# Performance work log

Hardware: AMD Instinct MI355X
Metric: run time of the kernel (lower is better)

Reference implementation:

```python
import jax, jax.numpy as jnp
import numpy as np

EPS = 1e-6

def _ln2d(x, g, b):
    # x: [b,H,W,c]; LayerNorm2d normalizes over channel dim per spatial location
    mu = jnp.mean(x, axis=-1, keepdims=True)
    var = jnp.mean((x - mu) ** 2, axis=-1, keepdims=True)
    return (x - mu) * jax.lax.rsqrt(var + EPS) * g + b

def _proj(x, w, b):
    # 1x1 conv == channel matmul; w: [c_out, c_in]
    return jnp.einsum('bhwc,dc->bhwd', x, w) + b

def setup_inputs() -> dict:
    key = jax.random.key(0)
    ks = jax.random.split(key, 16)
    b, c, H, W = 8, 96, 128, 256
    s = 0.02
    return {
        'feat_l': jax.random.normal(ks[0], (b, H * W, c), jnp.float32),
        'feat_r': jax.random.normal(ks[1], (b, H * W, c), jnp.float32),
        'g_nl': jnp.ones((c,), jnp.float32),
        'b_nl': jnp.zeros((c,), jnp.float32),
        'g_nr': jnp.ones((c,), jnp.float32),
        'b_nr': jnp.zeros((c,), jnp.float32),
        'w_l1': jax.random.normal(ks[2], (c, c), jnp.float32) * s,
        'bias_l1': jax.random.normal(ks[3], (c,), jnp.float32) * s,
        'w_r1': jax.random.normal(ks[4], (c, c), jnp.float32) * s,
        'bias_r1': jax.random.normal(ks[5], (c,), jnp.float32) * s,
        'w_l2': jax.random.normal(ks[6], (c, c), jnp.float32) * s,
        'bias_l2': jax.random.normal(ks[7], (c,), jnp.float32) * s,
        'w_r2': jax.random.normal(ks[8], (c, c), jnp.float32) * s,
        'bias_r2': jax.random.normal(ks[9], (c,), jnp.float32) * s,
        'beta': jax.random.normal(ks[10], (c,), jnp.float32) * 0.1,
        'gamma': jax.random.normal(ks[11], (c,), jnp.float32) * 0.1,
        'H': 128,
        'W': 256,
    }

def reference(feat_l, feat_r, g_nl, b_nl, g_nr, b_nr,
              w_l1, bias_l1, w_r1, bias_r1, w_l2, bias_l2, w_r2, bias_r2,
              beta, gamma, H, W):
    b, _, c = feat_l.shape
    scale = c ** (-0.5)
    # work in channels-last [b,H,W,c] (equivalent to torch's NCHW + permutes)
    x_l = feat_l.reshape(b, H, W, c)
    x_r = feat_r.reshape(b, H, W, c)
    Q_l = _proj(_ln2d(x_l, g_nl, b_nl), w_l1, bias_l1)   # [b,H,W,c]
    Q_r = _proj(_ln2d(x_r, g_nr, b_nr), w_r1, bias_r1)   # [b,H,W,c]
    V_l = _proj(x_l, w_l2, bias_l2)
    V_r = _proj(x_r, w_r2, bias_r2)
    attn = jnp.einsum('bhwc,bhvc->bhwv', Q_l, Q_r) * scale  # [b,H,W_l,W_r]
    F_r2l = jnp.einsum('bhwv,bhvc->bhwc', jax.nn.softmax(attn, axis=-1), V_r)
    attn_t = jnp.swapaxes(attn, -1, -2)                      # [b,H,W_r,W_l]
    F_l2r = jnp.einsum('bhvw,bhwc->bhvc', jax.nn.softmax(attn_t, axis=-1), V_l)
    out_l = x_l + F_r2l * beta
    out_r = x_r + F_l2r * gamma
    return (out_l.reshape(b, H * W, c), out_r.reshape(b, H * W, c))
```

## Files before the change

### kernel.cpp

```cpp
#include <hip/hip_runtime.h>
#include <stdint.h>

#define C96   96
#define TOTEL 25165824L

typedef __attribute__((ext_vector_type(16))) float f32x16;
typedef __attribute__((ext_vector_type(8)))  short short8;

#define QL_OFF  0
#define QR_OFF  53248
#define XT0_OFF 106496
#define XT1_OFF 119808
#define VT0_OFF 133120
#define VT1_OFF 146944
#define W1Q_OFF 106496
#define W1K_OFF 126464
#define LDS_SZ  160768

#define MFMA32(a,b,c) __builtin_amdgcn_mfma_f32_32x32x16_bf16(a,b,c,0,0,0)

__device__ __forceinline__ uint32_t cvtpk(float lo, float hi) {
    uint32_t d;
    asm("v_cvt_pk_bf16_f32 %0, %1, %2" : "=v"(d) : "v"(lo), "v"(hi));
    return d;
}
__device__ __forceinline__ float bl(uint32_t u){ union{uint32_t i;float f;}a; a.i=u<<16;        return a.f; }
__device__ __forceinline__ float bh(uint32_t u){ union{uint32_t i;float f;}a; a.i=u&0xffff0000u; return a.f; }

union F8 { uint32_t u[4]; short8 s; uint4 q; };

template<int ITERS>
__device__ __forceinline__ void stage(const float* __restrict__ src, char* dst, int t) {
#pragma unroll
    for (int i = 0; i < ITERS; ++i) {
        const int idx4 = i * 512 + t;
        const float4 v = *(const float4*)(src + (size_t)idx4 * 4);
        const int r = idx4 / 24;
        const int c = (idx4 % 24) * 4;
        uint2 p; p.x = cvtpk(v.x, v.y); p.y = cvtpk(v.z, v.w);
        *(uint2*)(dst + r * 208 + c * 2) = p;
    }
}

__device__ __forceinline__ void stageW(const float* __restrict__ W, char* dst, int t) {
#pragma unroll
    for (int i = 0; i < 5; ++i) {
        const int idx4 = i * 512 + t;
        if (idx4 < 2304) {
            const float4 v = *(const float4*)(W + (size_t)idx4 * 4);
            const int r = idx4 / 24;
            const int c = (idx4 % 24) * 4;
            uint2 p; p.x = cvtpk(v.x, v.y); p.y = cvtpk(v.z, v.w);
            *(uint2*)(dst + r * 208 + c * 2) = p;
        }
    }
}

__device__ __forceinline__ void stats512(char* lds_, int t) {
    char* row = lds_ + ((t < 256) ? QL_OFF : QR_OFF) + (t & 255) * 208;
    float sm = 0.f, s2 = 0.f;
#pragma unroll
    for (int i = 0; i < 12; ++i) {
        F8 w; w.q = *(const uint4*)(row + i * 16);
#pragma unroll
        for (int j = 0; j < 4; ++j) {
            const float a = bl(w.u[j]), b = bh(w.u[j]);
            sm += a + b; s2 += a * a + b * b;
        }
    }
    const float mu = sm * (1.f / 96.f);
    float var = s2 * (1.f / 96.f) - mu * mu;
    var = fmaxf(var, 0.f);
    *(float2*)(row + 192) = make_float2(mu, rsqrtf(var + 1e-6f));
}

__device__ __forceinline__ void proj_inplace(char* lds_, int qoff, int woff,
    const float* __restrict__ gv, const float* __restrict__ bv,
    const float* __restrict__ bias1, float outscale, int wv, int l31, int s)
{
    char* row = lds_ + qoff + (wv * 32 + l31) * 208;
    const float2 st = *(const float2*)(row + 192);
    const float mu = st.x, rs = st.y;
    short8 bf[6];
#pragma unroll
    for (int kf = 0; kf < 6; ++kf) {
        const int c0 = kf * 16 + s * 8;
        F8 raw; raw.q = *(const uint4*)(row + c0 * 2);
        const float4 g0 = *(const float4*)(gv + c0);
        const float4 g1 = *(const float4*)(gv + c0 + 4);
        const float4 b0 = *(const float4*)(bv + c0);
        const float4 b1 = *(const float4*)(bv + c0 + 4);
        const float x0=bl(raw.u[0]),x1=bh(raw.u[0]),x2=bl(raw.u[1]),x3=bh(raw.u[1]);
        const float x4=bl(raw.u[2]),x5=bh(raw.u[2]),x6=bl(raw.u[3]),x7=bh(raw.u[3]);
        F8 o;
        o.u[0] = cvtpk((x0-mu)*rs*g0.x + b0.x, (x1-mu)*rs*g0.y + b0.y);
        o.u[1] = cvtpk((x2-mu)*rs*g0.z + b0.z, (x3-mu)*rs*g0.w + b0.w);
        o.u[2] = cvtpk((x4-mu)*rs*g1.x + b1.x, (x5-mu)*rs*g1.y + b1.y);
        o.u[3] = cvtpk((x6-mu)*rs*g1.z + b1.z, (x7-mu)*rs*g1.w + b1.w);
        bf[kf] = o.s;
    }
    f32x16 qa[3];
#pragma unroll
    for (int i = 0; i < 16; ++i) { qa[0][i] = 0.f; qa[1][i] = 0.f; qa[2][i] = 0.f; }
#pragma unroll
    for (int kf = 0; kf < 6; ++kf) {
#pragma unroll
        for (int mf = 0; mf < 3; ++mf) {
            const short8 af = *(const short8*)(lds_ + woff + (mf * 32 + l31) * 208 + kf * 32 + s * 16);
            qa[mf] = MFMA32(af, bf[kf], qa[mf]);
        }
    }
#pragma unroll
    for (int mf = 0; mf < 3; ++mf) {
#pragma unroll
        for (int blk = 0; blk < 4; ++blk) {
            const int d = mf * 32 + blk * 8 + s * 4;
            const float4 bb = *(const float4*)(bias1 + d);
            uint2 p;
            p.x = cvtpk((qa[mf][blk*4+0] + bb.x) * outscale, (qa[mf][blk*4+1] + bb.y) * outscale);
            p.y = cvtpk((qa[mf][blk*4+2] + bb.z) * outscale, (qa[mf][blk*4+3] + bb.w) * outscale);
            *(uint2*)(row + d * 2) = p;
        }
    }
}

__device__ __forceinline__ void vproj(char* lds_, int xt_off, int vt_off,
    const short8* wf, const float* __restrict__ B2, int mfv, int nfv, int l31, int s)
{
    f32x16 va;
#pragma unroll
    for (int i = 0; i < 16; ++i) va[i] = 0.f;
#pragma unroll
    for (int kf = 0; kf < 6; ++kf) {
        const short8 xb = *(const short8*)(lds_ + xt_off + (nfv * 32 + l31) * 208 + kf * 32 + s * 16);
        va = MFMA32(wf[kf], xb, va);
    }
    const int v = nfv * 32 + l31;
#pragma unroll
    for (int blk = 0; blk < 4; ++blk) {
        const int d = mfv * 32 + blk * 8 + s * 4;
        const float4 bb = *(const float4*)(B2 + d);
        *(uint16_t*)(lds_ + vt_off + (d+0) * 144 + v * 2) = (uint16_t)cvtpk(va[blk*4+0] + bb.x, 0.f);
        *(uint16_t*)(lds_ + vt_off + (d+1) * 144 + v * 2) = (uint16_t)cvtpk(va[blk*4+1] + bb.y, 0.f);
        *(uint16_t*)(lds_ + vt_off + (d+2) * 144 + v * 2) = (uint16_t)cvtpk(va[blk*4+2] + bb.z, 0.f);
        *(uint16_t*)(lds_ + vt_off + (d+3) * 144 + v * 2) = (uint16_t)cvtpk(va[blk*4+3] + bb.w, 0.f);
    }
}

__device__ __forceinline__ void scalc(const char* lds_, int koff, int vt,
                                      const short8* bq, int l31, int s, f32x16* sa)
{
#pragma unroll
    for (int i = 0; i < 16; ++i) { sa[0][i] = 0.f; sa[1][i] = 0.f; }
#pragma unroll
    for (int kf = 0; kf < 6; ++kf) {
        const short8 a0 = *(const short8*)(lds_ + koff + (vt * 64 +      l31) * 208 + kf * 32 + s * 16);
        const short8 a1 = *(const short8*)(lds_ + koff + (vt * 64 + 32 + l31) * 208 + kf * 32 + s * 16);
        sa[0] = MFMA32(a0, bq[kf], sa[0]);
        sa[1] = MFMA32(a1, bq[kf], sa[1]);
    }
}

extern "C" __global__ __launch_bounds__(512, 2) void scam_fused(
    const float* __restrict__ feat_l, const float* __restrict__ feat_r,
    const float* __restrict__ g_nl, const float* __restrict__ b_nl,
    const float* __restrict__ g_nr, const float* __restrict__ b_nr,
    const float* __restrict__ w_l1, const float* __restrict__ bias_l1,
    const float* __restrict__ w_r1, const float* __restrict__ bias_r1,
    const float* __restrict__ w_l2, const float* __restrict__ bias_l2,
    const float* __restrict__ w_r2, const float* __restrict__ bias_r2,
    const float* __restrict__ beta, const float* __restrict__ gamma,
    float* __restrict__ out)
{
    extern __shared__ char lds[];
    const int t    = threadIdx.x;
    const int wv   = t >> 6;
    const int lane = t & 63;
    const int l31  = lane & 31;
    const int s    = lane >> 5;
    const size_t eb = (size_t)blockIdx.x * (256 * C96);
    const float scale = 0.10206207261596577f;

    stage<12>(feat_l + eb, lds + QL_OFF, t);
    stage<12>(feat_r + eb, lds + QR_OFF, t);
    stageW(w_l1, lds + (0 ? W1K_OFF : W1Q_OFF), t);
    stageW(w_r1, lds + W1K_OFF, t);
    __syncthreads();
    stats512(lds, t);
    __syncthreads();
    proj_inplace(lds, QL_OFF, W1Q_OFF, g_nl, b_nl, bias_l1, scale, wv, l31, s);
    proj_inplace(lds, QR_OFF, W1K_OFF, g_nr, b_nr, bias_r1, 1.0f,  wv, l31, s);

    for (int dir = 0; dir < 2; ++dir) {
        const int qoff = dir ? QR_OFF : QL_OFF;
        const int koff = dir ? QL_OFF : QR_OFF;
        const float* Xk   = dir ? feat_l  : feat_r;
        const float* Xq   = dir ? feat_r  : feat_l;
        const float* W2   = dir ? w_l2    : w_r2;
        const float* B2   = dir ? bias_l2 : bias_r2;
        const float* mixv = dir ? gamma   : beta;

        short8 bq[6];
#pragma unroll
        for (int kf = 0; kf < 6; ++kf)
            bq[kf] = *(const short8*)(lds + qoff + (wv * 32 + l31) * 208 + kf * 32 + s * 16);

        short8 wf[6];
        const int mfv = wv % 3, nfv = wv / 3;
        if (wv < 6) {
#pragma unroll
            for (int kf = 0; kf < 6; ++kf) {
                const float* wp = W2 + (mfv * 32 + l31) * 96 + kf * 16 + s * 8;
                const float4 a0 = *(const float4*)wp;
                const float4 a1 = *(const float4*)(wp + 4);
                F8 af;
                af.u[0] = cvtpk(a0.x, a0.y); af.u[1] = cvtpk(a0.z, a0.w);
                af.u[2] = cvtpk(a1.x, a1.y); af.u[3] = cvtpk(a1.z, a1.w);
                wf[kf] = af.s;
            }
        }

        f32x16 O[3];
#pragma unroll
        for (int i = 0; i < 16; ++i) { O[0][i] = 0.f; O[1][i] = 0.f; O[2][i] = 0.f; }
        float m_run = -1e30f, l_run = 0.f;
        f32x16 sab[2][2];

        __syncthreads();
        stage<3>(Xk + eb, lds + XT0_OFF, t);
        __syncthreads();
        if (wv < 6) vproj(lds, XT0_OFF, VT0_OFF, wf, B2, mfv, nfv, l31, s);
        stage<3>(Xk + eb + 64 * 96, lds + XT1_OFF, t);
        __syncthreads();
        scalc(lds, koff, 0, bq, l31, s, sab[0]);

#pragma unroll
        for (int vt = 0; vt < 4; ++vt) {
            const int cb = vt & 1, nb = cb ^ 1;
            if (vt < 3) scalc(lds, koff, vt + 1, bq, l31, s, sab[nb]);

            f32x16* sa = sab[cb];
            float tm = -1e30f;
#pragma unroll
            for (int i = 0; i < 16; ++i) { tm = fmaxf(tm, sa[0][i]); tm = fmaxf(tm, sa[1][i]); }
            tm = fmaxf(tm, __shfl_xor(tm, 32));
            const float mn = fmaxf(m_run, tm);
            const float al = __expf(m_run - mn);
            float ps = 0.f;
#pragma unroll
            for (int i = 0; i < 16; ++i) {
                sa[0][i] = __expf(sa[0][i] - mn); ps += sa[0][i];
                sa[1][i] = __expf(sa[1][i] - mn); ps += sa[1][i];
            }
            ps += __shfl_xor(ps, 32);
            l_run = l_run * al + ps;
            m_run = mn;
            O[0] *= al; O[1] *= al; O[2] *= al;

            const int vtoff = cb ? VT1_OFF : VT0_OFF;
#pragma unroll
            for (int kk = 0; kk < 4; ++kk) {
                const int mf = kk >> 1, base = (kk & 1) * 8;
                const uint32_t A0 = cvtpk(sa[mf][base+0], sa[mf][base+1]);
                const uint32_t A1 = cvtpk(sa[mf][base+2], sa[mf][base+3]);
                const uint32_t B0 = cvtpk(sa[mf][base+4], sa[mf][base+5]);
                const uint32_t B1 = cvtpk(sa[mf][base+6], sa[mf][base+7]);
                const uint32_t rA0 = __shfl_xor(A0, 32);
                const uint32_t rA1 = __shfl_xor(A1, 32);
                const uint32_t rB0 = __shfl_xor(B0, 32);
                const uint32_t rB1 = __shfl_xor(B1, 32);
                F8 pb;
                pb.u[0] = s ? rB0 : A0;
                pb.u[1] = s ? rB1 : A1;
                pb.u[2] = s ? B0  : rA0;
                pb.u[3] = s ? B1  : rA1;
#pragma unroll
                for (int mf2 = 0; mf2 < 3; ++mf2) {
                    const short8 av = *(const short8*)(lds + vtoff + (mf2 * 32 + l31) * 144 + kk * 32 + s * 16);
                    O[mf2] = MFMA32(av, pb.s, O[mf2]);
                }
            }

            if (vt < 3) {
                __syncthreads();
                if (wv < 6) vproj(lds, nb ? XT1_OFF : XT0_OFF, nb ? VT1_OFF : VT0_OFF,
                                  wf, B2, mfv, nfv, l31, s);
                if (vt < 2) stage<3>(Xk + eb + (size_t)(vt + 2) * 64 * 96,
                                     lds + (cb ? XT1_OFF : XT0_OFF), t);
                __syncthreads();
            }
        }

        const float inv = 1.f / l_run;
        const size_t rowbase = eb + (size_t)(wv * 32 + l31) * 96;
        float* oo = out + (dir ? TOTEL : 0);
#pragma unroll
        for (int mf = 0; mf < 3; ++mf) {
#pragma unroll
            for (int blk = 0; blk < 4; ++blk) {
                const int d = mf * 32 + blk * 8 + s * 4;
                const float4 mx = *(const float4*)(mixv + d);
                const float4 xr = *(const float4*)(Xq + rowbase + d);
                float4 ov;
                ov.x = fmaf(O[mf][blk*4+0] * inv, mx.x, xr.x);
                ov.y = fmaf(O[mf][blk*4+1] * inv, mx.y, xr.y);
                ov.z = fmaf(O[mf][blk*4+2] * inv, mx.z, xr.z);
                ov.w = fmaf(O[mf][blk*4+3] * inv, mx.w, xr.w);
                *(float4*)(oo + rowbase + d) = ov;
            }
        }
    }
}

extern "C" void kernel_launch(void* const* d_in, const int* in_sizes, int n_in,
                              void* d_out, int out_size, void* d_ws, size_t ws_size,
                              hipStream_t stream) {
    const float* feat_l  = (const float*)d_in[0];
    const float* feat_r  = (const float*)d_in[1];
    const float* g_nl    = (const float*)d_in[2];
    const float* b_nl    = (const float*)d_in[3];
    const float* g_nr    = (const float*)d_in[4];
    const float* b_nr    = (const float*)d_in[5];
    const float* w_l1    = (const float*)d_in[6];
    const float* bias_l1 = (const float*)d_in[7];
    const float* w_r1    = (const float*)d_in[8];
    const float* bias_r1 = (const float*)d_in[9];
    const float* w_l2    = (const float*)d_in[10];
    const float* bias_l2 = (const float*)d_in[11];
    const float* w_r2    = (const float*)d_in[12];
    const float* bias_r2 = (const float*)d_in[13];
    const float* beta    = (const float*)d_in[14];
    const float* gamma   = (const float*)d_in[15];
    float* out = (float*)d_out;

    hipLaunchKernelGGL(scam_fused, dim3(1024), dim3(512), LDS_SZ, stream,
                       feat_l, feat_r, g_nl, b_nl, g_nr, b_nr,
                       w_l1, bias_l1, w_r1, bias_r1, w_l2, bias_l2, w_r2, bias_r2,
                       beta, gamma, out);
}
```

Measured before the change: 215.2 us.

## Software-pipeline attention loop with register-staged loads, exp2 softmax, lazy rescale, setprio

Unrolls the four-tile attention loop by hand and splits global staging into issue and commit steps, so loads of the next K/V tile are in flight during score computation, softmax and the PV matmul. This cuts the barriers per tile from two to one. Softmax now uses the raw v_exp_f32 instruction, with log2(e) folded into the Q scale, and skips the running-max rescale of O when the new max grows by at most 8. MFMA blocks are wrapped in s_setprio, and the residual input rows are prefetched before the last PV. The costs are higher register pressure from the held float4 loads and the xr prefetch, plus a new barrier after projection.

```diff
diff --git a/kernel.cpp b/kernel.cpp
--- a/kernel.cpp
+++ b/kernel.cpp
@@ -24,32 +24,49 @@
     asm("v_cvt_pk_bf16_f32 %0, %1, %2" : "=v"(d) : "v"(lo), "v"(hi));
     return d;
 }
+__device__ __forceinline__ float fexp2(float x) {
+    float r; asm("v_exp_f32 %0, %1" : "=v"(r) : "v"(x)); return r;
+}
 __device__ __forceinline__ float bl(uint32_t u){ union{uint32_t i;float f;}a; a.i=u<<16;        return a.f; }
 __device__ __forceinline__ float bh(uint32_t u){ union{uint32_t i;float f;}a; a.i=u&0xffff0000u; return a.f; }
 
 union F8 { uint32_t u[4]; short8 s; uint4 q; };
 
+__device__ __forceinline__ void stage_issue(const float* __restrict__ src, int t,
+                                            float4& a0, float4& a1, float4& a2) {
+    a0 = *(const float4*)(src + (size_t)(0 * 512 + t) * 4);
+    a1 = *(const float4*)(src + (size_t)(1 * 512 + t) * 4);
+    a2 = *(const float4*)(src + (size_t)(2 * 512 + t) * 4);
+}
+__device__ __forceinline__ void stage_commit(char* dst, int t,
+                                             const float4& a0, const float4& a1, const float4& a2) {
+#pragma unroll
+    for (int i = 0; i < 3; ++i) {
+        const float4 v = (i == 0) ? a0 : (i == 1) ? a1 : a2;
+        const int idx4 = i * 512 + t;
+        const int r = idx4 / 24, c = (idx4 % 24) * 4;
+        uint2 p; p.x = cvtpk(v.x, v.y); p.y = cvtpk(v.z, v.w);
+        *(uint2*)(dst + r * 208 + c * 2) = p;
+    }
+}
 template<int ITERS>
 __device__ __forceinline__ void stage(const float* __restrict__ src, char* dst, int t) {
 #pragma unroll
     for (int i = 0; i < ITERS; ++i) {
         const int idx4 = i * 512 + t;
         const float4 v = *(const float4*)(src + (size_t)idx4 * 4);
-        const int r = idx4 / 24;
-        const int c = (idx4 % 24) * 4;
+        const int r = idx4 / 24, c = (idx4 % 24) * 4;
         uint2 p; p.x = cvtpk(v.x, v.y); p.y = cvtpk(v.z, v.w);
         *(uint2*)(dst + r * 208 + c * 2) = p;
     }
 }
-
 __device__ __forceinline__ void stageW(const float* __restrict__ W, char* dst, int t) {
 #pragma unroll
     for (int i = 0; i < 5; ++i) {
         const int idx4 = i * 512 + t;
         if (idx4 < 2304) {
             const float4 v = *(const float4*)(W + (size_t)idx4 * 4);
-            const int r = idx4 / 24;
-            const int c = (idx4 % 24) * 4;
+            const int r = idx4 / 24, c = (idx4 % 24) * 4;
             uint2 p; p.x = cvtpk(v.x, v.y); p.y = cvtpk(v.z, v.w);
             *(uint2*)(dst + r * 208 + c * 2) = p;
         }
@@ -102,6 +119,7 @@
     f32x16 qa[3];
 #pragma unroll
     for (int i = 0; i < 16; ++i) { qa[0][i] = 0.f; qa[1][i] = 0.f; qa[2][i] = 0.f; }
+    __builtin_amdgcn_s_setprio(1);
 #pragma unroll
     for (int kf = 0; kf < 6; ++kf) {
 #pragma unroll
@@ -110,6 +128,7 @@
             qa[mf] = MFMA32(af, bf[kf], qa[mf]);
         }
     }
+    __builtin_amdgcn_s_setprio(0);
 #pragma unroll
     for (int mf = 0; mf < 3; ++mf) {
 #pragma unroll
@@ -130,11 +149,13 @@
     f32x16 va;
 #pragma unroll
     for (int i = 0; i < 16; ++i) va[i] = 0.f;
+    __builtin_amdgcn_s_setprio(1);
 #pragma unroll
     for (int kf = 0; kf < 6; ++kf) {
         const short8 xb = *(const short8*)(lds_ + xt_off + (nfv * 32 + l31) * 208 + kf * 32 + s * 16);
         va = MFMA32(wf[kf], xb, va);
     }
+    __builtin_amdgcn_s_setprio(0);
     const int v = nfv * 32 + l31;
 #pragma unroll
     for (int blk = 0; blk < 4; ++blk) {
@@ -152,6 +173,7 @@
 {
 #pragma unroll
     for (int i = 0; i < 16; ++i) { sa[0][i] = 0.f; sa[1][i] = 0.f; }
+    __builtin_amdgcn_s_setprio(1);
 #pragma unroll
     for (int kf = 0; kf < 6; ++kf) {
         const short8 a0 = *(const short8*)(lds_ + koff + (vt * 64 +      l31) * 208 + kf * 32 + s * 16);
@@ -159,6 +181,87 @@
         sa[0] = MFMA32(a0, bq[kf], sa[0]);
         sa[1] = MFMA32(a1, bq[kf], sa[1]);
     }
+    __builtin_amdgcn_s_setprio(0);
+}
+
+__device__ __forceinline__ void softmax_tile(f32x16* sa, f32x16* O, float& m_run, float& l_run)
+{
+    float t0=-1e30f,t1=-1e30f,t2=-1e30f,t3=-1e30f;
+#pragma unroll
+    for (int i = 0; i < 16; i += 4) {
+        t0 = fmaxf(t0, fmaxf(sa[0][i+0], sa[1][i+0]));
+        t1 = fmaxf(t1, fmaxf(sa[0][i+1], sa[1][i+1]));
+        t2 = fmaxf(t2, fmaxf(sa[0][i+2], sa[1][i+2]));
+        t3 = fmaxf(t3, fmaxf(sa[0][i+3], sa[1][i+3]));
+    }
+    float tm = fmaxf(fmaxf(t0,t1), fmaxf(t2,t3));
+    tm = fmaxf(tm, __shfl_xor(tm, 32));
+    if (__all(tm - m_run <= 8.f)) {
+        const float mb = m_run;
+        float p0=0.f,p1=0.f,p2=0.f,p3=0.f;
+#pragma unroll
+        for (int i = 0; i < 16; i += 4) {
+            sa[0][i+0]=fexp2(sa[0][i+0]-mb); p0+=sa[0][i+0];
+            sa[1][i+0]=fexp2(sa[1][i+0]-mb); p0+=sa[1][i+0];
+            sa[0][i+1]=fexp2(sa[0][i+1]-mb); p1+=sa[0][i+1];
+            sa[1][i+1]=fexp2(sa[1][i+1]-mb); p1+=sa[1][i+1];
+            sa[0][i+2]=fexp2(sa[0][i+2]-mb); p2+=sa[0][i+2];
+            sa[1][i+2]=fexp2(sa[1][i+2]-mb); p2+=sa[1][i+2];
+            sa[0][i+3]=fexp2(sa[0][i+3]-mb); p3+=sa[0][i+3];
+            sa[1][i+3]=fexp2(sa[1][i+3]-mb); p3+=sa[1][i+3];
+        }
+        float ps = (p0+p1)+(p2+p3);
+        ps += __shfl_xor(ps, 32);
+        l_run += ps;
+    } else {
+        const float mn = fmaxf(m_run, tm);
+        const float al = fexp2(m_run - mn);
+        float p0=0.f,p1=0.f,p2=0.f,p3=0.f;
+#pragma unroll
+        for (int i = 0; i < 16; i += 4) {
+            sa[0][i+0]=fexp2(sa[0][i+0]-mn); p0+=sa[0][i+0];
+            sa[1][i+0]=fexp2(sa[1][i+0]-mn); p0+=sa[1][i+0];
+            sa[0][i+1]=fexp2(sa[0][i+1]-mn); p1+=sa[0][i+1];
+            sa[1][i+1]=fexp2(sa[1][i+1]-mn); p1+=sa[1][i+1];
+            sa[0][i+2]=fexp2(sa[0][i+2]-mn); p2+=sa[0][i+2];
+            sa[1][i+2]=fexp2(sa[1][i+2]-mn); p2+=sa[1][i+2];
+            sa[0][i+3]=fexp2(sa[0][i+3]-mn); p3+=sa[0][i+3];
+            sa[1][i+3]=fexp2(sa[1][i+3]-mn); p3+=sa[1][i+3];
+        }
+        float ps = (p0+p1)+(p2+p3);
+        ps += __shfl_xor(ps, 32);
+        l_run = l_run * al + ps;
+        m_run = mn;
+        O[0] *= al; O[1] *= al; O[2] *= al;
+    }
+}
+
+__device__ __forceinline__ void pv(const char* lds_, int vtoff, f32x16* sa, f32x16* O, int l31, int s)
+{
+    __builtin_amdgcn_s_setprio(1);
+#pragma unroll
+    for (int kk = 0; kk < 4; ++kk) {
+        const int mf = kk >> 1, base = (kk & 1) * 8;
+        const uint32_t A0 = cvtpk(sa[mf][base+0], sa[mf][base+1]);
+        const uint32_t A1 = cvtpk(sa[mf][base+2], sa[mf][base+3]);
+        const uint32_t B0 = cvtpk(sa[mf][base+4], sa[mf][base+5]);
+        const uint32_t B1 = cvtpk(sa[mf][base+6], sa[mf][base+7]);
+        const uint32_t rA0 = __shfl_xor(A0, 32);
+        const uint32_t rA1 = __shfl_xor(A1, 32);
+        const uint32_t rB0 = __shfl_xor(B0, 32);
+        const uint32_t rB1 = __shfl_xor(B1, 32);
+        F8 pb;
+        pb.u[0] = s ? rB0 : A0;
+        pb.u[1] = s ? rB1 : A1;
+        pb.u[2] = s ? B0  : rA0;
+        pb.u[3] = s ? B1  : rA1;
+#pragma unroll
+        for (int mf2 = 0; mf2 < 3; ++mf2) {
+            const short8 av = *(const short8*)(lds_ + vtoff + (mf2 * 32 + l31) * 144 + kk * 32 + s * 16);
+            O[mf2] = MFMA32(av, pb.s, O[mf2]);
+        }
+    }
+    __builtin_amdgcn_s_setprio(0);
 }
 
 extern "C" __global__ __launch_bounds__(512, 2) void scam_fused(
@@ -179,17 +282,18 @@
     const int l31  = lane & 31;
     const int s    = lane >> 5;
     const size_t eb = (size_t)blockIdx.x * (256 * C96);
-    const float scale = 0.10206207261596577f;
+    const float scale = 0.10206207261596577f * 1.4426950408889634f;
 
     stage<12>(feat_l + eb, lds + QL_OFF, t);
     stage<12>(feat_r + eb, lds + QR_OFF, t);
-    stageW(w_l1, lds + (0 ? W1K_OFF : W1Q_OFF), t);
+    stageW(w_l1, lds + W1Q_OFF, t);
     stageW(w_r1, lds + W1K_OFF, t);
     __syncthreads();
     stats512(lds, t);
     __syncthreads();
     proj_inplace(lds, QL_OFF, W1Q_OFF, g_nl, b_nl, bias_l1, scale, wv, l31, s);
     proj_inplace(lds, QR_OFF, W1K_OFF, g_nr, b_nr, bias_r1, 1.0f,  wv, l31, s);
+    __syncthreads();
 
     for (int dir = 0; dir < 2; ++dir) {
         const int qoff = dir ? QR_OFF : QL_OFF;
@@ -199,6 +303,9 @@
         const float* W2   = dir ? w_l2    : w_r2;
         const float* B2   = dir ? bias_l2 : bias_r2;
         const float* mixv = dir ? gamma   : beta;
+
+        float4 A0, A1, A2;
+        stage_issue(Xk + eb, t, A0, A1, A2);
 
         short8 bq[6];
 #pragma unroll
@@ -220,79 +327,50 @@
             }
         }
 
+        stage_commit(lds + XT0_OFF, t, A0, A1, A2);
+        __syncthreads();
+        if (wv < 6) vproj(lds, XT0_OFF, VT0_OFF, wf, B2, mfv, nfv, l31, s);
+        stage_issue(Xk + eb + 64 * 96, t, A0, A1, A2);
+        stage_commit(lds + XT1_OFF, t, A0, A1, A2);
+        __syncthreads();
+
         f32x16 O[3];
 #pragma unroll
         for (int i = 0; i < 16; ++i) { O[0][i] = 0.f; O[1][i] = 0.f; O[2][i] = 0.f; }
         float m_run = -1e30f, l_run = 0.f;
-        f32x16 sab[2][2];
-
+        f32x16 sa0[2], sa1[2];
+        scalc(lds, koff, 0, bq, l31, s, sa0);
+
+        stage_issue(Xk + eb + 2 * 64 * 96, t, A0, A1, A2);
+        scalc(lds, koff, 1, bq, l31, s, sa1);
+        softmax_tile(sa0, O, m_run, l_run);
+        if (wv < 6) vproj(lds, XT1_OFF, VT1_OFF, wf, B2, mfv, nfv, l31, s);
+        pv(lds, VT0_OFF, sa0, O, l31, s);
+        stage_commit(lds + XT0_OFF, t, A0, A1, A2);
         __syncthreads();
-        stage<3>(Xk + eb, lds + XT0_OFF, t);
+        stage_issue(Xk + eb + 3 * 64 * 96, t, A0, A1, A2);
+        scalc(lds, koff, 2, bq, l31, s, sa0);
+        softmax_tile(sa1, O, m_run, l_run);
+        if (wv < 6) vproj(lds, XT0_OFF, VT0_OFF, wf, B2, mfv, nfv, l31, s);
+        pv(lds, VT1_OFF, sa1, O, l31, s);
+        stage_commit(lds + XT1_OFF, t, A0, A1, A2);
         __syncthreads();
-        if (wv < 6) vproj(lds, XT0_OFF, VT0_OFF, wf, B2, mfv, nfv, l31, s);
-        stage<3>(Xk + eb + 64 * 96, lds + XT1_OFF, t);
+        scalc(lds, koff, 3, bq, l31, s, sa1);
+        softmax_tile(sa0, O, m_run, l_run);
+        if (wv < 6) vproj(lds, XT1_OFF, VT1_OFF, wf, B2, mfv, nfv, l31, s);
+        pv(lds, VT0_OFF, sa0, O, l31, s);
         __syncthreads();
-        scalc(lds, koff, 0, bq, l31, s, sab[0]);
-
-#pragma unroll
-        for (int vt = 0; vt < 4; ++vt) {
-            const int cb = vt & 1, nb = cb ^ 1;
-            if (vt < 3) scalc(lds, koff, vt + 1, bq, l31, s, sab[nb]);
-
-            f32x16* sa = sab[cb];
-            float tm = -1e30f;
-#pragma unroll
-            for (int i = 0; i < 16; ++i) { tm = fmaxf(tm, sa[0][i]); tm = fmaxf(tm, sa[1][i]); }
-            tm = fmaxf(tm, __shfl_xor(tm, 32));
-            const float mn = fmaxf(m_run, tm);
-            const float al = __expf(m_run - mn);
-            float ps = 0.f;
-#pragma unroll
-            for (int i = 0; i < 16; ++i) {
-                sa[0][i] = __expf(sa[0][i] - mn); ps += sa[0][i];
-                sa[1][i] = __expf(sa[1][i] - mn); ps += sa[1][i];
-            }
-            ps += __shfl_xor(ps, 32);
-            l_run = l_run * al + ps;
-            m_run = mn;
-            O[0] *= al; O[1] *= al; O[2] *= al;
-
-            const int vtoff = cb ? VT1_OFF : VT0_OFF;
-#pragma unroll
-            for (int kk = 0; kk < 4; ++kk) {
-                const int mf = kk >> 1, base = (kk & 1) * 8;
-                const uint32_t A0 = cvtpk(sa[mf][base+0], sa[mf][base+1]);
-                const uint32_t A1 = cvtpk(sa[mf][base+2], sa[mf][base+3]);
-                const uint32_t B0 = cvtpk(sa[mf][base+4], sa[mf][base+5]);
-                const uint32_t B1 = cvtpk(sa[mf][base+6], sa[mf][base+7]);
-                const uint32_t rA0 = __shfl_xor(A0, 32);
-                const uint32_t rA1 = __shfl_xor(A1, 32);
-                const uint32_t rB0 = __shfl_xor(B0, 32);
-                const uint32_t rB1 = __shfl_xor(B1, 32);
-                F8 pb;
-                pb.u[0] = s ? rB0 : A0;
-                pb.u[1] = s ? rB1 : A1;
-                pb.u[2] = s ? B0  : rA0;
-                pb.u[3] = s ? B1  : rA1;
-#pragma unroll
-                for (int mf2 = 0; mf2 < 3; ++mf2) {
-                    const short8 av = *(const short8*)(lds + vtoff + (mf2 * 32 + l31) * 144 + kk * 32 + s * 16);
-                    O[mf2] = MFMA32(av, pb.s, O[mf2]);
-                }
-            }
-
-            if (vt < 3) {
-                __syncthreads();
-                if (wv < 6) vproj(lds, nb ? XT1_OFF : XT0_OFF, nb ? VT1_OFF : VT0_OFF,
-                                  wf, B2, mfv, nfv, l31, s);
-                if (vt < 2) stage<3>(Xk + eb + (size_t)(vt + 2) * 64 * 96,
-                                     lds + (cb ? XT1_OFF : XT0_OFF), t);
-                __syncthreads();
-            }
-        }
+        softmax_tile(sa1, O, m_run, l_run);
+        const size_t rowbase = eb + (size_t)(wv * 32 + l31) * 96;
+        float4 xr[12];
+#pragma unroll
+        for (int mf = 0; mf < 3; ++mf)
+#pragma unroll
+            for (int blk = 0; blk < 4; ++blk)
+                xr[mf*4+blk] = *(const float4*)(Xq + rowbase + mf * 32 + blk * 8 + s * 4);
+        pv(lds, VT1_OFF, sa1, O, l31, s);
 
         const float inv = 1.f / l_run;
-        const size_t rowbase = eb + (size_t)(wv * 32 + l31) * 96;
         float* oo = out + (dir ? TOTEL : 0);
 #pragma unroll
         for (int mf = 0; mf < 3; ++mf) {
@@ -300,12 +378,12 @@
             for (int blk = 0; blk < 4; ++blk) {
                 const int d = mf * 32 + blk * 8 + s * 4;
                 const float4 mx = *(const float4*)(mixv + d);
-                const float4 xr = *(const float4*)(Xq + rowbase + d);
+                const float4 rv = xr[mf*4+blk];
                 float4 ov;
-                ov.x = fmaf(O[mf][blk*4+0] * inv, mx.x, xr.x);
-                ov.y = fmaf(O[mf][blk*4+1] * inv, mx.y, xr.y);
-                ov.z = fmaf(O[mf][blk*4+2] * inv, mx.z, xr.z);
-                ov.w = fmaf(O[mf][blk*4+3] * inv, mx.w, xr.w);
+                ov.x = fmaf(O[mf][blk*4+0] * inv, mx.x, rv.x);
+                ov.y = fmaf(O[mf][blk*4+1] * inv, mx.y, rv.y);
+                ov.z = fmaf(O[mf][blk*4+2] * inv, mx.z, rv.z);
+                ov.w = fmaf(O[mf][blk*4+3] * inv, mx.w, rv.w);
                 *(float4*)(oo + rowbase + d) = ov;
             }
         }
```

New measurement: 296.0 us. +37.5%, slower.

## Use exp2 softmax with deferred max rescale and MFMA priority hints

Applied to the files above, without the earlier changes.

Folds log2(e) into the query projection scale so the online softmax can call the raw v_exp_f32 (base-2) instruction instead of __expf. It skips the running-max update and the O/l rescale when no lane's tile max exceeds the running max by more than 8. It also splits the max and sum reductions into four independent chains and wraps the MFMA loops with s_setprio so matrix work gets issue priority over other waves. Deferring the rescale leaves exponentials up to 2^8 in bf16 P and fp32 accumulators, which is safe for these magnitudes but slightly changes numerics.

```diff
diff --git a/kernel.cpp b/kernel.cpp
--- a/kernel.cpp
+++ b/kernel.cpp
@@ -24,6 +24,9 @@
     asm("v_cvt_pk_bf16_f32 %0, %1, %2" : "=v"(d) : "v"(lo), "v"(hi));
     return d;
 }
+__device__ __forceinline__ float fexp2(float x) {
+    float r; asm("v_exp_f32 %0, %1" : "=v"(r) : "v"(x)); return r;
+}
 __device__ __forceinline__ float bl(uint32_t u){ union{uint32_t i;float f;}a; a.i=u<<16;        return a.f; }
 __device__ __forceinline__ float bh(uint32_t u){ union{uint32_t i;float f;}a; a.i=u&0xffff0000u; return a.f; }
 
@@ -35,21 +38,18 @@
     for (int i = 0; i < ITERS; ++i) {
         const int idx4 = i * 512 + t;
         const float4 v = *(const float4*)(src + (size_t)idx4 * 4);
-        const int r = idx4 / 24;
-        const int c = (idx4 % 24) * 4;
+        const int r = idx4 / 24, c = (idx4 % 24) * 4;
         uint2 p; p.x = cvtpk(v.x, v.y); p.y = cvtpk(v.z, v.w);
         *(uint2*)(dst + r * 208 + c * 2) = p;
     }
 }
-
 __device__ __forceinline__ void stageW(const float* __restrict__ W, char* dst, int t) {
 #pragma unroll
     for (int i = 0; i < 5; ++i) {
         const int idx4 = i * 512 + t;
         if (idx4 < 2304) {
             const float4 v = *(const float4*)(W + (size_t)idx4 * 4);
-            const int r = idx4 / 24;
-            const int c = (idx4 % 24) * 4;
+            const int r = idx4 / 24, c = (idx4 % 24) * 4;
             uint2 p; p.x = cvtpk(v.x, v.y); p.y = cvtpk(v.z, v.w);
             *(uint2*)(dst + r * 208 + c * 2) = p;
         }
@@ -102,6 +102,7 @@
     f32x16 qa[3];
 #pragma unroll
     for (int i = 0; i < 16; ++i) { qa[0][i] = 0.f; qa[1][i] = 0.f; qa[2][i] = 0.f; }
+    __builtin_amdgcn_s_setprio(1);
 #pragma unroll
     for (int kf = 0; kf < 6; ++kf) {
 #pragma unroll
@@ -110,6 +111,7 @@
             qa[mf] = MFMA32(af, bf[kf], qa[mf]);
         }
     }
+    __builtin_amdgcn_s_setprio(0);
 #pragma unroll
     for (int mf = 0; mf < 3; ++mf) {
 #pragma unroll
@@ -130,11 +132,13 @@
     f32x16 va;
 #pragma unroll
     for (int i = 0; i < 16; ++i) va[i] = 0.f;
+    __builtin_amdgcn_s_setprio(1);
 #pragma unroll
     for (int kf = 0; kf < 6; ++kf) {
         const short8 xb = *(const short8*)(lds_ + xt_off + (nfv * 32 + l31) * 208 + kf * 32 + s * 16);
         va = MFMA32(wf[kf], xb, va);
     }
+    __builtin_amdgcn_s_setprio(0);
     const int v = nfv * 32 + l31;
 #pragma unroll
     for (int blk = 0; blk < 4; ++blk) {
@@ -152,6 +156,7 @@
 {
 #pragma unroll
     for (int i = 0; i < 16; ++i) { sa[0][i] = 0.f; sa[1][i] = 0.f; }
+    __builtin_amdgcn_s_setprio(1);
 #pragma unroll
     for (int kf = 0; kf < 6; ++kf) {
         const short8 a0 = *(const short8*)(lds_ + koff + (vt * 64 +      l31) * 208 + kf * 32 + s * 16);
@@ -159,6 +164,73 @@
         sa[0] = MFMA32(a0, bq[kf], sa[0]);
         sa[1] = MFMA32(a1, bq[kf], sa[1]);
     }
+    __builtin_amdgcn_s_setprio(0);
+}
+
+__device__ __forceinline__ void softmax_tile(f32x16* sa, f32x16* O, float& m_run, float& l_run)
+{
+    float t0=-1e30f,t1=-1e30f,t2=-1e30f,t3=-1e30f;
+#pragma unroll
+    for (int i = 0; i < 16; i += 4) {
+        t0 = fmaxf(t0, fmaxf(sa[0][i+0], sa[1][i+0]));
+        t1 = fmaxf(t1, fmaxf(sa[0][i+1], sa[1][i+1]));
+        t2 = fmaxf(t2, fmaxf(sa[0][i+2], sa[1][i+2]));
+        t3 = fmaxf(t3, fmaxf(sa[0][i+3], sa[1][i+3]));
+    }
+    float tm = fmaxf(fmaxf(t0,t1), fmaxf(t2,t3));
+    tm = fmaxf(tm, __shfl_xor(tm, 32));
+    const bool defer = __all(tm - m_run <= 8.f);
+    const float mn = defer ? m_run : fmaxf(m_run, tm);
+    float p0=0.f,p1=0.f,p2=0.f,p3=0.f;
+#pragma unroll
+    for (int i = 0; i < 16; i += 4) {
+        sa[0][i+0]=fexp2(sa[0][i+0]-mn); p0+=sa[0][i+0];
+        sa[1][i+0]=fexp2(sa[1][i+0]-mn); p0+=sa[1][i+0];
+        sa[0][i+1]=fexp2(sa[0][i+1]-mn); p1+=sa[0][i+1];
+        sa[1][i+1]=fexp2(sa[1][i+1]-mn); p1+=sa[1][i+1];
+        sa[0][i+2]=fexp2(sa[0][i+2]-mn); p2+=sa[0][i+2];
+        sa[1][i+2]=fexp2(sa[1][i+2]-mn); p2+=sa[1][i+2];
+        sa[0][i+3]=fexp2(sa[0][i+3]-mn); p3+=sa[0][i+3];
+        sa[1][i+3]=fexp2(sa[1][i+3]-mn); p3+=sa[1][i+3];
+    }
+    float ps = (p0+p1)+(p2+p3);
+    ps += __shfl_xor(ps, 32);
+    if (defer) {
+        l_run += ps;
+    } else {
+        const float al = fexp2(m_run - mn);
+        l_run = l_run * al + ps;
+        m_run = mn;
+        O[0] *= al; O[1] *= al; O[2] *= al;
+    }
+}
+
+__device__ __forceinline__ void pv(const char* lds_, int vtoff, f32x16* sa, f32x16* O, int l31, int s)
+{
+    __builtin_amdgcn_s_setprio(1);
+#pragma unroll
+    for (int kk = 0; kk < 4; ++kk) {
+        const int mf = kk >> 1, base = (kk & 1) * 8;
+        const uint32_t A0 = cvtpk(sa[mf][base+0], sa[mf][base+1]);
+        const uint32_t A1 = cvtpk(sa[mf][base+2], sa[mf][base+3]);
+        const uint32_t B0 = cvtpk(sa[mf][base+4], sa[mf][base+5]);
+        const uint32_t B1 = cvtpk(sa[mf][base+6], sa[mf][base+7]);
+        const uint32_t rA0 = __shfl_xor(A0, 32);
+        const uint32_t rA1 = __shfl_xor(A1, 32);
+        const uint32_t rB0 = __shfl_xor(B0, 32);
+        const uint32_t rB1 = __shfl_xor(B1, 32);
+        F8 pb;
+        pb.u[0] = s ? rB0 : A0;
+        pb.u[1] = s ? rB1 : A1;
+        pb.u[2] = s ? B0  : rA0;
+        pb.u[3] = s ? B1  : rA1;
+#pragma unroll
+        for (int mf2 = 0; mf2 < 3; ++mf2) {
+            const short8 av = *(const short8*)(lds_ + vtoff + (mf2 * 32 + l31) * 144 + kk * 32 + s * 16);
+            O[mf2] = MFMA32(av, pb.s, O[mf2]);
+        }
+    }
+    __builtin_amdgcn_s_setprio(0);
 }
 
 extern "C" __global__ __launch_bounds__(512, 2) void scam_fused(
@@ -179,11 +251,11 @@
     const int l31  = lane & 31;
     const int s    = lane >> 5;
     const size_t eb = (size_t)blockIdx.x * (256 * C96);
-    const float scale = 0.10206207261596577f;
+    const float scale = 0.10206207261596577f * 1.4426950408889634f;
 
     stage<12>(feat_l + eb, lds + QL_OFF, t);
     stage<12>(feat_r + eb, lds + QR_OFF, t);
-    stageW(w_l1, lds + (0 ? W1K_OFF : W1Q_OFF), t);
+    stageW(w_l1, lds + W1Q_OFF, t);
     stageW(w_r1, lds + W1K_OFF, t);
     __syncthreads();
     stats512(lds, t);
@@ -240,46 +312,9 @@
             if (vt < 3) scalc(lds, koff, vt + 1, bq, l31, s, sab[nb]);
 
             f32x16* sa = sab[cb];
-            float tm = -1e30f;
-#pragma unroll
-            for (int i = 0; i < 16; ++i) { tm = fmaxf(tm, sa[0][i]); tm = fmaxf(tm, sa[1][i]); }
-            tm = fmaxf(tm, __shfl_xor(tm, 32));
-            const float mn = fmaxf(m_run, tm);
-            const float al = __expf(m_run - mn);
-            float ps = 0.f;
-#pragma unroll
-            for (int i = 0; i < 16; ++i) {
-                sa[0][i] = __expf(sa[0][i] - mn); ps += sa[0][i];
-                sa[1][i] = __expf(sa[1][i] - mn); ps += sa[1][i];
-            }
-            ps += __shfl_xor(ps, 32);
-            l_run = l_run * al + ps;
-            m_run = mn;
-            O[0] *= al; O[1] *= al; O[2] *= al;
-
-            const int vtoff = cb ? VT1_OFF : VT0_OFF;
-#pragma unroll
-            for (int kk = 0; kk < 4; ++kk) {
-                const int mf = kk >> 1, base = (kk & 1) * 8;
-                const uint32_t A0 = cvtpk(sa[mf][base+0], sa[mf][base+1]);
-                const uint32_t A1 = cvtpk(sa[mf][base+2], sa[mf][base+3]);
-                const uint32_t B0 = cvtpk(sa[mf][base+4], sa[mf][base+5]);
-                const uint32_t B1 = cvtpk(sa[mf][base+6], sa[mf][base+7]);
-                const uint32_t rA0 = __shfl_xor(A0, 32);
-                const uint32_t rA1 = __shfl_xor(A1, 32);
-                const uint32_t rB0 = __shfl_xor(B0, 32);
-                const uint32_t rB1 = __shfl_xor(B1, 32);
-                F8 pb;
-                pb.u[0] = s ? rB0 : A0;
-                pb.u[1] = s ? rB1 : A1;
-                pb.u[2] = s ? B0  : rA0;
-                pb.u[3] = s ? B1  : rA1;
-#pragma unroll
-                for (int mf2 = 0; mf2 < 3; ++mf2) {
-                    const short8 av = *(const short8*)(lds + vtoff + (mf2 * 32 + l31) * 144 + kk * 32 + s * 16);
-                    O[mf2] = MFMA32(av, pb.s, O[mf2]);
-                }
-            }
+            softmax_tile(sa, O, m_run, l_run);
+
+            pv(lds, cb ? VT1_OFF : VT0_OFF, sa, O, l31, s);
 
             if (vt < 3) {
                 __syncthreads();
```

After: 226.4 us. 1.05x slower.

## Compute full V projection upfront from global memory, drop pipelined staging

Applied to the files above, without the earlier changes.

Instead of double-buffering 64-row tiles of the key-side input through LDS and computing V projections tile by tile between softmax steps, each direction now computes the full 256-row V^T into a single LDS buffer at the start. The work is spread across all 8 waves, with X and W read directly from global memory. The attention loop then processes 32-key halves with no barriers inside. This removes several __syncthreads per direction and the idle waves during vproj. In exchange it loses the overlap of V computation with attention, and the score accumulator shrinks to one tile per step, which may reduce MFMA ILP.

```diff
diff --git a/kernel.cpp b/kernel.cpp
--- a/kernel.cpp
+++ b/kernel.cpp
@@ -7,15 +7,14 @@
 typedef __attribute__((ext_vector_type(16))) float f32x16;
 typedef __attribute__((ext_vector_type(8)))  short short8;
 
-#define QL_OFF  0
-#define QR_OFF  53248
-#define XT0_OFF 106496
-#define XT1_OFF 119808
-#define VT0_OFF 133120
-#define VT1_OFF 146944
+#define QROWB  208
+#define VROWB  528
+#define QL_OFF 0
+#define QR_OFF 53248
+#define VT_OFF 106496
 #define W1Q_OFF 106496
 #define W1K_OFF 126464
-#define LDS_SZ  160768
+#define LDS_SZ 157184
 
 #define MFMA32(a,b,c) __builtin_amdgcn_mfma_f32_32x32x16_bf16(a,b,c,0,0,0)
 
@@ -35,29 +34,26 @@
     for (int i = 0; i < ITERS; ++i) {
         const int idx4 = i * 512 + t;
         const float4 v = *(const float4*)(src + (size_t)idx4 * 4);
-        const int r = idx4 / 24;
-        const int c = (idx4 % 24) * 4;
+        const int r = idx4 / 24, c = (idx4 % 24) * 4;
         uint2 p; p.x = cvtpk(v.x, v.y); p.y = cvtpk(v.z, v.w);
-        *(uint2*)(dst + r * 208 + c * 2) = p;
-    }
-}
-
+        *(uint2*)(dst + r * QROWB + c * 2) = p;
+    }
+}
 __device__ __forceinline__ void stageW(const float* __restrict__ W, char* dst, int t) {
 #pragma unroll
     for (int i = 0; i < 5; ++i) {
         const int idx4 = i * 512 + t;
         if (idx4 < 2304) {
             const float4 v = *(const float4*)(W + (size_t)idx4 * 4);
-            const int r = idx4 / 24;
-            const int c = (idx4 % 24) * 4;
+            const int r = idx4 / 24, c = (idx4 % 24) * 4;
             uint2 p; p.x = cvtpk(v.x, v.y); p.y = cvtpk(v.z, v.w);
-            *(uint2*)(dst + r * 208 + c * 2) = p;
+            *(uint2*)(dst + r * QROWB + c * 2) = p;
         }
     }
 }
 
 __device__ __forceinline__ void stats512(char* lds_, int t) {
-    char* row = lds_ + ((t < 256) ? QL_OFF : QR_OFF) + (t & 255) * 208;
+    char* row = lds_ + ((t < 256) ? QL_OFF : QR_OFF) + (t & 255) * QROWB;
     float sm = 0.f, s2 = 0.f;
 #pragma unroll
     for (int i = 0; i < 12; ++i) {
@@ -78,7 +74,7 @@
     const float* __restrict__ gv, const float* __restrict__ bv,
     const float* __restrict__ bias1, float outscale, int wv, int l31, int s)
 {
-    char* row = lds_ + qoff + (wv * 32 + l31) * 208;
+    char* row = lds_ + qoff + (wv * 32 + l31) * QROWB;
     const float2 st = *(const float2*)(row + 192);
     const float mu = st.x, rs = st.y;
     short8 bf[6];
@@ -106,7 +102,7 @@
     for (int kf = 0; kf < 6; ++kf) {
 #pragma unroll
         for (int mf = 0; mf < 3; ++mf) {
-            const short8 af = *(const short8*)(lds_ + woff + (mf * 32 + l31) * 208 + kf * 32 + s * 16);
+            const short8 af = *(const short8*)(lds_ + woff + (mf * 32 + l31) * QROWB + kf * 32 + s * 16);
             qa[mf] = MFMA32(af, bf[kf], qa[mf]);
         }
     }
@@ -124,40 +120,39 @@
     }
 }
 
-__device__ __forceinline__ void vproj(char* lds_, int xt_off, int vt_off,
-    const short8* wf, const float* __restrict__ B2, int mfv, int nfv, int l31, int s)
+__device__ __forceinline__ void vproj_job(char* lds_, const float* __restrict__ Xk,
+    const float* __restrict__ W2, const float* __restrict__ B2,
+    size_t eb, int job, int l31, int s)
 {
+    const int mf = job % 3, v0 = (job / 3) * 32;
     f32x16 va;
 #pragma unroll
     for (int i = 0; i < 16; ++i) va[i] = 0.f;
 #pragma unroll
     for (int kf = 0; kf < 6; ++kf) {
-        const short8 xb = *(const short8*)(lds_ + xt_off + (nfv * 32 + l31) * 208 + kf * 32 + s * 16);
-        va = MFMA32(wf[kf], xb, va);
-    }
-    const int v = nfv * 32 + l31;
+        const int c0 = kf * 16 + s * 8;
+        const float* xp = Xk + eb + (size_t)(v0 + l31) * 96 + c0;
+        const float4 x0 = *(const float4*)xp;
+        const float4 x1 = *(const float4*)(xp + 4);
+        F8 xb;
+        xb.u[0] = cvtpk(x0.x, x0.y); xb.u[1] = cvtpk(x0.z, x0.w);
+        xb.u[2] = cvtpk(x1.x, x1.y); xb.u[3] = cvtpk(x1.z, x1.w);
+        const float* wp = W2 + (mf * 32 + l31) * 96 + c0;
+        const float4 a0 = *(const float4*)wp;
+        const float4 a1 = *(const float4*)(wp + 4);
+        F8 af;
+        af.u[0] = cvtpk(a0.x, a0.y); af.u[1] = cvtpk(a0.z, a0.w);
+        af.u[2] = cvtpk(a1.x, a1.y); af.u[3] = cvtpk(a1.z, a1.w);
+        va = MFMA32(af.s, xb.s, va);
+    }
 #pragma unroll
     for (int blk = 0; blk < 4; ++blk) {
-        const int d = mfv * 32 + blk * 8 + s * 4;
+        const int d = mf * 32 + blk * 8 + s * 4;
         const float4 bb = *(const float4*)(B2 + d);
-        *(uint16_t*)(lds_ + vt_off + (d+0) * 144 + v * 2) = (uint16_t)cvtpk(va[blk*4+0] + bb.x, 0.f);
-        *(uint16_t*)(lds_ + vt_off + (d+1) * 144 + v * 2) = (uint16_t)cvtpk(va[blk*4+1] + bb.y, 0.f);
-        *(uint16_t*)(lds_ + vt_off + (d+2) * 144 + v * 2) = (uint16_t)cvtpk(va[blk*4+2] + bb.z, 0.f);
-        *(uint16_t*)(lds_ + vt_off + (d+3) * 144 + v * 2) = (uint16_t)cvtpk(va[blk*4+3] + bb.w, 0.f);
-    }
-}
-
-__device__ __forceinline__ void scalc(const char* lds_, int koff, int vt,
-                                      const short8* bq, int l31, int s, f32x16* sa)
-{
-#pragma unroll
-    for (int i = 0; i < 16; ++i) { sa[0][i] = 0.f; sa[1][i] = 0.f; }
-#pragma unroll
-    for (int kf = 0; kf < 6; ++kf) {
-        const short8 a0 = *(const short8*)(lds_ + koff + (vt * 64 +      l31) * 208 + kf * 32 + s * 16);
-        const short8 a1 = *(const short8*)(lds_ + koff + (vt * 64 + 32 + l31) * 208 + kf * 32 + s * 16);
-        sa[0] = MFMA32(a0, bq[kf], sa[0]);
-        sa[1] = MFMA32(a1, bq[kf], sa[1]);
+        *(uint16_t*)(lds_ + VT_OFF + (d+0) * VROWB + (v0 + l31) * 2) = (uint16_t)cvtpk(va[blk*4+0] + bb.x, 0.f);
+        *(uint16_t*)(lds_ + VT_OFF + (d+1) * VROWB + (v0 + l31) * 2) = (uint16_t)cvtpk(va[blk*4+1] + bb.y, 0.f);
+        *(uint16_t*)(lds_ + VT_OFF + (d+2) * VROWB + (v0 + l31) * 2) = (uint16_t)cvtpk(va[blk*4+2] + bb.z, 0.f);
+        *(uint16_t*)(lds_ + VT_OFF + (d+3) * VROWB + (v0 + l31) * 2) = (uint16_t)cvtpk(va[blk*4+3] + bb.w, 0.f);
     }
 }
 
@@ -183,13 +178,14 @@
 
     stage<12>(feat_l + eb, lds + QL_OFF, t);
     stage<12>(feat_r + eb, lds + QR_OFF, t);
-    stageW(w_l1, lds + (0 ? W1K_OFF : W1Q_OFF), t);
+    stageW(w_l1, lds + W1Q_OFF, t);
     stageW(w_r1, lds + W1K_OFF, t);
     __syncthreads();
     stats512(lds, t);
     __syncthreads();
     proj_inplace(lds, QL_OFF, W1Q_OFF, g_nl, b_nl, bias_l1, scale, wv, l31, s);
     proj_inplace(lds, QR_OFF, W1K_OFF, g_nr, b_nr, bias_r1, 1.0f,  wv, l31, s);
+    __syncthreads();
 
     for (int dir = 0; dir < 2; ++dir) {
         const int qoff = dir ? QR_OFF : QL_OFF;
@@ -200,71 +196,53 @@
         const float* B2   = dir ? bias_l2 : bias_r2;
         const float* mixv = dir ? gamma   : beta;
 
+#pragma unroll
+        for (int i = 0; i < 3; ++i)
+            vproj_job(lds, Xk, W2, B2, eb, wv + 8 * i, l31, s);
+        __syncthreads();
+
         short8 bq[6];
 #pragma unroll
         for (int kf = 0; kf < 6; ++kf)
-            bq[kf] = *(const short8*)(lds + qoff + (wv * 32 + l31) * 208 + kf * 32 + s * 16);
-
-        short8 wf[6];
-        const int mfv = wv % 3, nfv = wv / 3;
-        if (wv < 6) {
-#pragma unroll
-            for (int kf = 0; kf < 6; ++kf) {
-                const float* wp = W2 + (mfv * 32 + l31) * 96 + kf * 16 + s * 8;
-                const float4 a0 = *(const float4*)wp;
-                const float4 a1 = *(const float4*)(wp + 4);
-                F8 af;
-                af.u[0] = cvtpk(a0.x, a0.y); af.u[1] = cvtpk(a0.z, a0.w);
-                af.u[2] = cvtpk(a1.x, a1.y); af.u[3] = cvtpk(a1.z, a1.w);
-                wf[kf] = af.s;
-            }
-        }
+            bq[kf] = *(const short8*)(lds + qoff + (wv * 32 + l31) * QROWB + kf * 32 + s * 16);
 
         f32x16 O[3];
 #pragma unroll
         for (int i = 0; i < 16; ++i) { O[0][i] = 0.f; O[1][i] = 0.f; O[2][i] = 0.f; }
         float m_run = -1e30f, l_run = 0.f;
-        f32x16 sab[2][2];
-
-        __syncthreads();
-        stage<3>(Xk + eb, lds + XT0_OFF, t);
-        __syncthreads();
-        if (wv < 6) vproj(lds, XT0_OFF, VT0_OFF, wf, B2, mfv, nfv, l31, s);
-        stage<3>(Xk + eb + 64 * 96, lds + XT1_OFF, t);
-        __syncthreads();
-        scalc(lds, koff, 0, bq, l31, s, sab[0]);
-
-#pragma unroll
-        for (int vt = 0; vt < 4; ++vt) {
-            const int cb = vt & 1, nb = cb ^ 1;
-            if (vt < 3) scalc(lds, koff, vt + 1, bq, l31, s, sab[nb]);
-
-            f32x16* sa = sab[cb];
+
+#pragma unroll
+        for (int step = 0; step < 8; ++step) {
+            const int vt = step >> 1, half = step & 1;
+            f32x16 sa;
+#pragma unroll
+            for (int i = 0; i < 16; ++i) sa[i] = 0.f;
+#pragma unroll
+            for (int kf = 0; kf < 6; ++kf) {
+                const short8 a0 = *(const short8*)(lds + koff +
+                    (vt * 64 + half * 32 + l31) * QROWB + kf * 32 + s * 16);
+                sa = MFMA32(a0, bq[kf], sa);
+            }
             float tm = -1e30f;
 #pragma unroll
-            for (int i = 0; i < 16; ++i) { tm = fmaxf(tm, sa[0][i]); tm = fmaxf(tm, sa[1][i]); }
+            for (int i = 0; i < 16; ++i) tm = fmaxf(tm, sa[i]);
             tm = fmaxf(tm, __shfl_xor(tm, 32));
             const float mn = fmaxf(m_run, tm);
             const float al = __expf(m_run - mn);
             float ps = 0.f;
 #pragma unroll
-            for (int i = 0; i < 16; ++i) {
-                sa[0][i] = __expf(sa[0][i] - mn); ps += sa[0][i];
-                sa[1][i] = __expf(sa[1][i] - mn); ps += sa[1][i];
-            }
+            for (int i = 0; i < 16; ++i) { sa[i] = __expf(sa[i] - mn); ps += sa[i]; }
             ps += __shfl_xor(ps, 32);
             l_run = l_run * al + ps;
             m_run = mn;
             O[0] *= al; O[1] *= al; O[2] *= al;
-
-            const int vtoff = cb ? VT1_OFF : VT0_OFF;
-#pragma unroll
-            for (int kk = 0; kk < 4; ++kk) {
-                const int mf = kk >> 1, base = (kk & 1) * 8;
-                const uint32_t A0 = cvtpk(sa[mf][base+0], sa[mf][base+1]);
-                const uint32_t A1 = cvtpk(sa[mf][base+2], sa[mf][base+3]);
-                const uint32_t B0 = cvtpk(sa[mf][base+4], sa[mf][base+5]);
-                const uint32_t B1 = cvtpk(sa[mf][base+6], sa[mf][base+7]);
+#pragma unroll
+            for (int kc = 0; kc < 2; ++kc) {
+                const int base = kc * 8;
+                const uint32_t A0 = cvtpk(sa[base+0], sa[base+1]);
+                const uint32_t A1 = cvtpk(sa[base+2], sa[base+3]);
+                const uint32_t B0 = cvtpk(sa[base+4], sa[base+5]);
+                const uint32_t B1 = cvtpk(sa[base+6], sa[base+7]);
                 const uint32_t rA0 = __shfl_xor(A0, 32);
                 const uint32_t rA1 = __shfl_xor(A1, 32);
                 const uint32_t rB0 = __shfl_xor(B0, 32);
@@ -276,18 +254,10 @@
                 pb.u[3] = s ? B1  : rA1;
 #pragma unroll
                 for (int mf2 = 0; mf2 < 3; ++mf2) {
-                    const short8 av = *(const short8*)(lds + vtoff + (mf2 * 32 + l31) * 144 + kk * 32 + s * 16);
+                    const short8 av = *(const short8*)(lds + VT_OFF +
+                        (mf2 * 32 + l31) * VROWB + vt * 128 + half * 64 + kc * 32 + s * 16);
                     O[mf2] = MFMA32(av, pb.s, O[mf2]);
                 }
-            }
-
-            if (vt < 3) {
-                __syncthreads();
-                if (wv < 6) vproj(lds, nb ? XT1_OFF : XT0_OFF, nb ? VT1_OFF : VT0_OFF,
-                                  wf, B2, mfv, nfv, l31, s);
-                if (vt < 2) stage<3>(Xk + eb + (size_t)(vt + 2) * 64 * 96,
-                                     lds + (cb ? XT1_OFF : XT0_OFF), t);
-                __syncthreads();
             }
         }
 
@@ -309,6 +279,7 @@
                 *(float4*)(oo + rowbase + d) = ov;
             }
         }
+        if (dir == 0) __syncthreads();
     }
 }
 
```

Result: slower. 327.6 us (+52.2%).
